# Performance work log

Hardware: AMD Instinct MI355X
Metric: run time of the kernel (lower is better)

## Reference

```python
import jax, jax.numpy as jnp
import numpy as np

B, S, D, DFF = 4, 2048, 1024, 4096
EPS = 1e-5


def layernorm(x, gamma, beta):
    mu = jnp.mean(x, axis=-1, keepdims=True)
    var = jnp.var(x, axis=-1, keepdims=True)
    return (x - mu) * jax.lax.rsqrt(var + EPS) * gamma + beta


def attention(Q, K, V, causal):
    d_k = Q.shape[-1]
    scores = jnp.einsum('bqd,bkd->bqk', Q, K) / jnp.sqrt(jnp.asarray(d_k, Q.dtype))
    if causal:
        q_len, k_len = scores.shape[-2], scores.shape[-1]
        mask = jnp.tril(jnp.ones((q_len, k_len), dtype=bool))
        scores = jnp.where(mask[None], scores, jnp.asarray(-jnp.inf, scores.dtype))
    w = jax.nn.softmax(scores, axis=-1)
    return jnp.einsum('bqk,bkd->bqd', w, V)


def setup_inputs() -> dict:
    key = jax.random.key(0)
    ks = jax.random.split(key, 12)
    sd = 0.02
    return {
        'y': jax.random.normal(ks[0], (B, S, D), jnp.float32),
        'Z': jax.random.normal(ks[1], (B, S, D), jnp.float32),
        'w1': jax.random.normal(ks[2], (D, DFF), jnp.float32) * sd,
        'b1': jnp.zeros((DFF,), jnp.float32),
        'w2': jax.random.normal(ks[3], (DFF, D), jnp.float32) * sd,
        'b2': jnp.zeros((D,), jnp.float32),
        'g1': jnp.ones((D,), jnp.float32), 'beta1': jnp.zeros((D,), jnp.float32),
        'g2': jnp.ones((D,), jnp.float32), 'beta2': jnp.zeros((D,), jnp.float32),
        'g3': jnp.ones((D,), jnp.float32), 'beta3': jnp.zeros((D,), jnp.float32),
    }


def reference(y, Z, w1, b1, w2, b2, g1, beta1, g2, beta2, g3, beta3):
    # masked (causal) self-attention, single head over full d_model
    sa = attention(y, y, y, causal=True)
    y = layernorm(y + sa, g1, beta1)
    # cross-attention to encoder memory Z
    ca = attention(y, Z, Z, causal=False)
    y = layernorm(y + ca, g2, beta2)
    # position-wise FFN
    h = jax.nn.relu(jnp.einsum('bsd,df->bsf', y, w1) + b1)
    ff = jnp.einsum('bsf,fd->bsd', h, w2) + b2
    y = layernorm(y + ff, g3, beta3)
    return y
```

## Files before the change

kernel.cpp:

```cpp
#include <hip/hip_runtime.h>
#include <hip/hip_bf16.h>


#define Bb 4
#define Ss 2048
#define Dd 1024
#define Ff 4096

typedef __attribute__((ext_vector_type(4))) float f32x4;
typedef __attribute__((ext_vector_type(8))) short bf16x8;
typedef __attribute__((ext_vector_type(8))) unsigned short u16x8;
typedef __attribute__((ext_vector_type(4))) unsigned short u16x4;

__device__ __forceinline__ unsigned short f2bf(float f) {
  unsigned u = __float_as_uint(f);
  u += 0x7FFFu + ((u >> 16) & 1u);
  return (unsigned short)(u >> 16);
}
__device__ __forceinline__ float bf2f(unsigned short h) {
  return __uint_as_float(((unsigned)h) << 16);
}

__device__ __forceinline__ void gload_lds16(const void* g, void* l) {
  __builtin_amdgcn_global_load_lds((const __attribute__((address_space(1))) void*)g,
                                   (__attribute__((address_space(3))) void*)l, 16, 0, 0);
}

__device__ __forceinline__ int xcd8(int orig, int n) {
  int q = n >> 3, r = n & 7;
  int x = orig & 7;
  int base = x < r ? x * (q + 1) : r * (q + 1) + (x - r) * q;
  return base + (orig >> 3);
}

__global__ __launch_bounds__(256) void k_transpose_cast(const float* __restrict__ in,
                                                        unsigned short* __restrict__ outT,
                                                        unsigned short* __restrict__ outR,
                                                        int R, int C) {
  __shared__ float t[32][33];
  size_t bo = (size_t)blockIdx.z * R * C;
  const float* pin = in + bo;
  unsigned short* poutT = outT + bo;
  unsigned short* poutR = outR ? outR + bo : nullptr;
  int c0 = blockIdx.x * 32, r0 = blockIdx.y * 32;
  int tx = threadIdx.x, ty = threadIdx.y;
#pragma unroll
  for (int i = 0; i < 4; i++) {
    float v = pin[(size_t)(r0 + ty + i * 8) * C + c0 + tx];
    t[ty + i * 8][tx] = v;
    if (poutR) poutR[(size_t)(r0 + ty + i * 8) * C + c0 + tx] = f2bf(v);
  }
  __syncthreads();
#pragma unroll
  for (int i = 0; i < 4; i++)
    poutT[(size_t)(c0 + ty + i * 8) * R + r0 + tx] = f2bf(t[tx][ty + i * 8]);
}

#define BAR() __builtin_amdgcn_s_barrier()
#define PRIO1() __builtin_amdgcn_s_setprio(1)
#define PRIO0() __builtin_amdgcn_s_setprio(0)
#define LGKM0()                                          \
  {                                                      \
    asm volatile("s_waitcnt lgkmcnt(0)" ::: "memory");   \
    __builtin_amdgcn_sched_barrier(0);                   \
  }

#define LDA8(arr, mh, bo)                                                       \
  {                                                                             \
    _Pragma("unroll") for (int j_ = 0; j_ < QM; ++j_) {                         \
      _Pragma("unroll") for (int kh_ = 0; kh_ < 2; ++kh_) {                     \
        arr[j_][kh_] =                                                          \
            *(const bf16x8*)(lds + (bo) + ((mh)*QM + j_) * 2048 + aof[kh_]);    \
      }                                                                         \
    }                                                                           \
  }

#define LDB8(arr, nh, bo)                                                       \
  {                                                                             \
    _Pragma("unroll") for (int n_ = 0; n_ < 2; ++n_) {                          \
      _Pragma("unroll") for (int kh_ = 0; kh_ < 2; ++kh_) {                     \
        arr[n_][kh_] =                                                          \
            *(const bf16x8*)(lds + (bo) + ((nh)*2 + n_) * 2048 + bof[kh_]);     \
      }                                                                         \
    }                                                                           \
  }

#define MMQ(aarr, barr, mh, nh)                                                 \
  {                                                                             \
    _Pragma("unroll") for (int j_ = 0; j_ < QM; ++j_) {                         \
      _Pragma("unroll") for (int n_ = 0; n_ < 2; ++n_) {                        \
        _Pragma("unroll") for (int kh_ = 0; kh_ < 2; ++kh_) {                   \
          acc[(mh)*QM + j_][(nh)*2 + n_] = __builtin_amdgcn_mfma_f32_16x16x32_bf16( \
              aarr[j_][kh_], barr[n_][kh_], acc[(mh)*QM + j_][(nh)*2 + n_], 0, 0, 0); \
        }                                                                       \
      }                                                                         \
    }                                                                           \
  }

#define EPILOGUE(MR_, WMS_)                                                     \
  {                                                                             \
    const int colb = j0 + wc * 64 + fr;                                         \
    const int rowb = i0 + wr * (WMS_) + (kq << 2);                              \
    const size_t cb = (size_t)bz * bsC;                                         \
    _Pragma("unroll") for (int m = 0; m < (MR_); ++m) {                         \
      _Pragma("unroll") for (int r = 0; r < 4; ++r) {                           \
        size_t ro = cb + (size_t)(rowb + m * 16 + r) * ldc;                     \
        _Pragma("unroll") for (int n = 0; n < 4; ++n) {                         \
          float v = acc[m][n][r];                                               \
          int col = colb + n * 16;                                              \
          if (EPI == 0) Cb[ro + col] = f2bf(v * scale);                         \
          else if (EPI == 2) Cb[ro + col] = f2bf(fmaxf(v + bias[col], 0.f));    \
          else if (EPI == 4) Cf[ro + col] = v + resid[ro + col];                \
          else Cf[ro + col] = v + bias[col] + resid[ro + col];                  \
        }                                                                       \
      }                                                                         \
    }                                                                           \
  }

template <int EPI, bool CAUSAL>
__global__ __launch_bounds__(512) void k_gemm8(
    const unsigned short* __restrict__ Ag, const unsigned short* __restrict__ Bg,
    float* __restrict__ Cf, unsigned short* __restrict__ Cb,
    const float* __restrict__ bias, const float* __restrict__ resid,
    int K, int lda, int ldb, int ldc, long bsA, long bsB, long bsC, float scale) {
  constexpr int QM = 4;
  constexpr int ABYTES = 32768, BBYTES = 32768;
  __shared__ alignas(16) char lds[2 * ABYTES + 2 * BBYTES];

  int i0, j0;
  if (CAUSAL) {
    int t = xcd8(blockIdx.x, gridDim.x);
    int ti = (int)((sqrtf(8.f * t + 1.f) - 1.f) * 0.5f);
    while ((ti + 1) * (ti + 2) / 2 <= t) ++ti;
    while (ti * (ti + 1) / 2 > t) --ti;
    i0 = ti * 256;
    j0 = (t - ti * (ti + 1) / 2) * 256;
  } else {
    int lin = xcd8(blockIdx.y * gridDim.x + blockIdx.x, gridDim.x * gridDim.y);
    i0 = (lin / gridDim.x) * 256;
    j0 = (lin % gridDim.x) * 256;
  }
  int bz = blockIdx.z;
  Ag += (size_t)bz * bsA;
  Bg += (size_t)bz * bsB;

  const int nk = K / 64;
  const int niter = nk / 2;

  const int tid = threadIdx.x;
  const int w = tid >> 6, lane = tid & 63;
  const int wr = w >> 2, wc = w & 3;

  const int srow = (w << 3) + (lane >> 3);
  const int bcs = (lane & 7) ^ (lane >> 3);
  const unsigned short* As = Ag + (size_t)(i0 + srow) * lda + bcs * 8;
  const unsigned short* Bs = Bg + (size_t)(j0 + srow) * ldb + bcs * 8;
  char* ldsAw = lds + w * 1024;
  char* ldsBw = lds + 2 * ABYTES + w * 1024;

  auto stA = [&](int kt, int hf) {
    int ks = kt < nk ? kt : nk - 1;
#pragma unroll
    for (int l = 0; l < 2; ++l)
      gload_lds16(As + (size_t)(hf * 128 + l * 64) * lda + ks * 64,
                  ldsAw + (kt & 1) * ABYTES + hf * 128 * 128 + l * 8192);
  };
  auto stB = [&](int kt, int hf) {
    int ks = kt < nk ? kt : nk - 1;
#pragma unroll
    for (int l = 0; l < 2; ++l)
      gload_lds16(Bs + (size_t)(hf * 128 + l * 64) * ldb + ks * 64,
                  ldsBw + (kt & 1) * BBYTES + hf * 128 * 128 + l * 8192);
  };

  const int fr = lane & 15, kq = lane >> 4;
  const int rA = wr * 128 + fr;
  const int rB = wc * 64 + fr;
  unsigned aof[2], bof[2];
  aof[0] = rA * 128 + ((kq ^ (rA & 7)) << 4);
  aof[1] = rA * 128 + (((kq + 4) ^ (rA & 7)) << 4);
  bof[0] = 2 * ABYTES + rB * 128 + ((kq ^ (rB & 7)) << 4);
  bof[1] = 2 * ABYTES + rB * 128 + (((kq + 4) ^ (rB & 7)) << 4);
  constexpr int A0 = 0, A1 = ABYTES, B0 = 0, B1 = BBYTES;

  f32x4 acc[8][4];
#pragma unroll
  for (int m = 0; m < 8; ++m)
#pragma unroll
    for (int n = 0; n < 4; ++n) acc[m][n] = (f32x4){0.f, 0.f, 0.f, 0.f};

  bf16x8 a0[QM][2], a1[QM][2], b0[2][2], b1[2][2];

  stA(0, 0); stA(0, 1); stB(0, 0); stB(0, 1);
  stA(1, 0); stA(1, 1); stB(1, 0);
  asm volatile("s_waitcnt vmcnt(6)" ::: "memory");
  BAR();
  LDB8(b0, 0, B0);

  for (int t = 0; t < niter; ++t) {
    const int ka = 2 * t + 2, kb = 2 * t + 3;
    LDA8(a0, 0, A0);
    stB(2 * t + 1, 1);
    BAR(); LGKM0(); PRIO1(); MMQ(a0, b0, 0, 0); PRIO0(); BAR();
    LDA8(a1, 1, A0);
    BAR(); LGKM0(); PRIO1(); MMQ(a1, b0, 1, 0); PRIO0(); BAR();
    LDB8(b1, 1, B0);
    stA(ka, 0);
    asm volatile("s_waitcnt vmcnt(2)" ::: "memory");
    BAR(); LGKM0(); PRIO1(); MMQ(a1, b1, 1, 1); PRIO0(); BAR();
    LDB8(b0, 0, B1);
    stA(ka, 1); stB(ka, 0);
    BAR(); LGKM0(); PRIO1(); MMQ(a0, b1, 0, 1); PRIO0(); BAR();
    LDA8(a0, 0, A1);
    stB(ka, 1);
    BAR(); LGKM0(); PRIO1(); MMQ(a0, b0, 0, 0); PRIO0(); BAR();
    LDA8(a1, 1, A1);
    BAR(); LGKM0(); PRIO1(); MMQ(a1, b0, 1, 0); PRIO0(); BAR();
    LDB8(b1, 1, B1);
    stA(kb, 0);
    asm volatile("s_waitcnt vmcnt(2)" ::: "memory");
    BAR(); LGKM0(); PRIO1(); MMQ(a1, b1, 1, 1); PRIO0(); BAR();
    LDB8(b0, 0, B0);
    stA(kb, 1); stB(kb, 0);
    BAR(); LGKM0(); PRIO1(); MMQ(a0, b1, 0, 1); PRIO0(); BAR();
  }
  EPILOGUE(8, 128)
}

template <int EPI, bool KCAP>
__global__ __launch_bounds__(512) void k_gemm4(
    const unsigned short* __restrict__ Ag, const unsigned short* __restrict__ Bg,
    float* __restrict__ Cf, unsigned short* __restrict__ Cb,
    const float* __restrict__ bias, const float* __restrict__ resid,
    int K, int lda, int ldb, int ldc, long bsA, long bsB, long bsC, float scale) {
  constexpr int QM = 4;
  constexpr int ABYTES = 16384, BBYTES = 32768;
  __shared__ alignas(16) char lds[2 * ABYTES + 2 * BBYTES];

  int lin = xcd8(blockIdx.y * gridDim.x + blockIdx.x, gridDim.x * gridDim.y);
  int i0 = (lin / gridDim.x) * 128;
  int j0 = (lin % gridDim.x) * 256;
  int bz = blockIdx.z;
  Ag += (size_t)bz * bsA;
  Bg += (size_t)bz * bsB;

  int nk = K / 64;
  if (KCAP) {
    int cap = i0 / 64 + 2;
    nk = nk < cap ? nk : cap;
  }
  const int niter = nk / 2;

  const int tid = threadIdx.x;
  const int w = tid >> 6, lane = tid & 63;
  const int wr = w >> 2, wc = w & 3;

  const int srow = (w << 3) + (lane >> 3);
  const int bcs = (lane & 7) ^ (lane >> 3);
  const unsigned short* As = Ag + (size_t)(i0 + srow) * lda + bcs * 8;
  const unsigned short* Bs = Bg + (size_t)(j0 + srow) * ldb + bcs * 8;
  char* ldsAw = lds + w * 1024;
  char* ldsBw = lds + 2 * ABYTES + w * 1024;

  auto stA2 = [&](int kt) {
    int ks = kt < nk ? kt : nk - 1;
#pragma unroll
    for (int hf = 0; hf < 2; ++hf)
      gload_lds16(As + (size_t)(hf * 64) * lda + ks * 64,
                  ldsAw + (kt & 1) * ABYTES + hf * 64 * 128);
  };
  auto stB2 = [&](int kt) {
    int ks = kt < nk ? kt : nk - 1;
#pragma unroll
    for (int hf = 0; hf < 2; ++hf)
#pragma unroll
      for (int l = 0; l < 2; ++l)
        gload_lds16(Bs + (size_t)(hf * 128 + l * 64) * ldb + ks * 64,
                    ldsBw + (kt & 1) * BBYTES + hf * 128 * 128 + l * 8192);
  };

  const int fr = lane & 15, kq = lane >> 4;
  const int rA = wr * 64 + fr;
  const int rB = wc * 64 + fr;
  unsigned aof[2], bof[2];
  aof[0] = rA * 128 + ((kq ^ (rA & 7)) << 4);
  aof[1] = rA * 128 + (((kq + 4) ^ (rA & 7)) << 4);
  bof[0] = 2 * ABYTES + rB * 128 + ((kq ^ (rB & 7)) << 4);
  bof[1] = 2 * ABYTES + rB * 128 + (((kq + 4) ^ (rB & 7)) << 4);
  constexpr int A0 = 0, A1 = ABYTES, B0 = 0, B1 = BBYTES;

  f32x4 acc[4][4];
#pragma unroll
  for (int m = 0; m < 4; ++m)
#pragma unroll
    for (int n = 0; n < 4; ++n) acc[m][n] = (f32x4){0.f, 0.f, 0.f, 0.f};

  bf16x8 a[QM][2], b0[2][2], b1[2][2];

  stA2(0); stB2(0); stA2(1);
  asm volatile("s_waitcnt vmcnt(2)" ::: "memory");
  BAR();

  for (int t = 0; t < niter; ++t) {
    const int ka = 2 * t + 2, kb = 2 * t + 3;
    LDA8(a, 0, A0); LDB8(b0, 0, B0);
    stB2(2 * t + 1);
    BAR(); LGKM0(); PRIO1(); MMQ(a, b0, 0, 0); PRIO0(); BAR();
    LDB8(b1, 1, B0);
    stA2(ka);
    asm volatile("s_waitcnt vmcnt(2)" ::: "memory");
    BAR(); LGKM0(); PRIO1(); MMQ(a, b1, 0, 1); PRIO0(); BAR();
    LDA8(a, 0, A1); LDB8(b0, 0, B1);
    stB2(ka);
    BAR(); LGKM0(); PRIO1(); MMQ(a, b0, 0, 0); PRIO0(); BAR();
    LDB8(b1, 1, B1);
    stA2(kb);
    asm volatile("s_waitcnt vmcnt(2)" ::: "memory");
    BAR(); LGKM0(); PRIO1(); MMQ(a, b1, 0, 1); PRIO0(); BAR();
  }
  EPILOGUE(4, 64)
}

template <bool CAUSAL>
__global__ __launch_bounds__(256) void k_softmax(unsigned short* __restrict__ scores) {
  int row = blockIdx.x;
  int i = row & (Ss - 1);
  unsigned short* src = scores + (size_t)row * Ss;
  int nv = CAUSAL ? i + 1 : Ss;
  int nb = CAUSAL ? ((i & ~127) + 128) : Ss;
  int t = threadIdx.x;
  int w = t >> 6, lane = t & 63;
  bool act = t * 8 < nb;
  float v[8];
  float mx = -1e30f;
  if (act) {
    u16x8 raw = *(const u16x8*)(src + t * 8);
#pragma unroll
    for (int k = 0; k < 8; k++) {
      int j = t * 8 + k;
      v[k] = (j < nv) ? bf2f(raw[k]) : -1e30f;
      mx = fmaxf(mx, v[k]);
    }
  } else {
#pragma unroll
    for (int k = 0; k < 8; k++) v[k] = -1e30f;
  }
#pragma unroll
  for (int o = 32; o; o >>= 1) mx = fmaxf(mx, __shfl_xor(mx, o));
  __shared__ float red[8];
  if (lane == 0) red[w] = mx;
  __syncthreads();
  mx = fmaxf(fmaxf(red[0], red[1]), fmaxf(red[2], red[3]));
  float sum = 0.f;
#pragma unroll
  for (int k = 0; k < 8; k++) {
    float e = (v[k] > -1e29f) ? __expf(v[k] - mx) : 0.f;
    v[k] = e;
    sum += e;
  }
#pragma unroll
  for (int o = 32; o; o >>= 1) sum += __shfl_xor(sum, o);
  if (lane == 0) red[4 + w] = sum;
  __syncthreads();
  sum = red[4] + red[5] + red[6] + red[7];
  float inv = 1.f / sum;
  if (act) {
    u16x8 r;
#pragma unroll
    for (int k = 0; k < 8; k++) r[k] = f2bf(v[k] * inv);
    *(u16x8*)(src + t * 8) = r;
  }
}

__global__ __launch_bounds__(256) void k_ln(const float* __restrict__ a,
                                            const float* __restrict__ g,
                                            const float* __restrict__ be,
                                            float* __restrict__ outf,
                                            unsigned short* __restrict__ outb) {
  int row = blockIdx.x;
  size_t o = (size_t)row * Dd;
  int t = threadIdx.x;
  f32x4 x = *(const f32x4*)(a + o + t * 4);
  float s = x[0] + x[1] + x[2] + x[3];
  float q = x[0] * x[0] + x[1] * x[1] + x[2] * x[2] + x[3] * x[3];
  int w = t >> 6, lane = t & 63;
#pragma unroll
  for (int of = 32; of; of >>= 1) {
    s += __shfl_xor(s, of);
    q += __shfl_xor(q, of);
  }
  __shared__ float red[8];
  if (lane == 0) {
    red[w] = s;
    red[4 + w] = q;
  }
  __syncthreads();
  s = red[0] + red[1] + red[2] + red[3];
  q = red[4] + red[5] + red[6] + red[7];
  float mean = s * (1.f / Dd);
  float var = q * (1.f / Dd) - mean * mean;
  float rstd = rsqrtf(var + 1e-5f);
  f32x4 gv = *(const f32x4*)(g + t * 4);
  f32x4 bv = *(const f32x4*)(be + t * 4);
  f32x4 y;
#pragma unroll
  for (int k = 0; k < 4; k++) y[k] = (x[k] - mean) * rstd * gv[k] + bv[k];
  *(f32x4*)(outf + o + t * 4) = y;
  if (outb) {
    u16x4 r;
    r[0] = f2bf(y[0]); r[1] = f2bf(y[1]); r[2] = f2bf(y[2]); r[3] = f2bf(y[3]);
    *(u16x4*)(outb + o + t * 4) = r;
  }
}

extern "C" void kernel_launch(void* const* d_in, const int* in_sizes, int n_in, void* d_out,
                              int out_size, void* d_ws, size_t ws_size, hipStream_t stream) {
  (void)in_sizes; (void)n_in; (void)out_size; (void)ws_size;
  const float* y   = (const float*)d_in[0];
  const float* Z   = (const float*)d_in[1];
  const float* w1  = (const float*)d_in[2];
  const float* b1  = (const float*)d_in[3];
  const float* w2  = (const float*)d_in[4];
  const float* b2  = (const float*)d_in[5];
  const float* g1  = (const float*)d_in[6];
  const float* be1 = (const float*)d_in[7];
  const float* g2  = (const float*)d_in[8];
  const float* be2 = (const float*)d_in[9];
  const float* g3  = (const float*)d_in[10];
  const float* be3 = (const float*)d_in[11];
  float* out = (float*)d_out;

  char* ws = (char*)d_ws;
  const size_t MB = 1024ull * 1024ull;
  unsigned short* T   = (unsigned short*)(ws);
  unsigned short* Zbf = (unsigned short*)(ws + 16 * MB);
  unsigned short* ybf = (unsigned short*)(ws + 32 * MB);
  unsigned short* w1t = (unsigned short*)(ws + 48 * MB);
  unsigned short* w2t = (unsigned short*)(ws + 56 * MB);
  unsigned short* sc  = (unsigned short*)(ws + 64 * MB);
  unsigned short* h   = (unsigned short*)(ws + 64 * MB);
  float* res          = (float*)(ws + 128 * MB);
  float* attn         = (float*)d_out;

  dim3 b256(256), b512(512);
  const float scl = 1.f / 32.f;

  k_transpose_cast<<<dim3(Dd / 32, Ss / 32, Bb), dim3(32, 8), 0, stream>>>(y, T, ybf, Ss, Dd);
  k_gemm8<0, true><<<dim3(36, 1, Bb), b512, 0, stream>>>(
      ybf, ybf, nullptr, sc, nullptr, nullptr, Dd, Dd, Dd, Ss,
      (long)Ss * Dd, (long)Ss * Dd, (long)Ss * Ss, scl);
  k_softmax<true><<<dim3(Bb * Ss), b256, 0, stream>>>(sc);
  k_gemm4<4, true><<<dim3(Dd / 256, Ss / 128, Bb), b512, 0, stream>>>(
      sc, T, attn, nullptr, nullptr, y, Ss, Ss, Ss, Dd,
      (long)Ss * Ss, (long)Dd * Ss, (long)Ss * Dd, 1.f);
  k_ln<<<dim3(Bb * Ss), b256, 0, stream>>>(attn, g1, be1, res, ybf);

  k_transpose_cast<<<dim3(Dd / 32, Ss / 32, Bb), dim3(32, 8), 0, stream>>>(Z, T, Zbf, Ss, Dd);
  k_gemm8<0, false><<<dim3(Ss / 256, Ss / 256, Bb), b512, 0, stream>>>(
      ybf, Zbf, nullptr, sc, nullptr, nullptr, Dd, Dd, Dd, Ss,
      (long)Ss * Dd, (long)Ss * Dd, (long)Ss * Ss, scl);
  k_softmax<false><<<dim3(Bb * Ss), b256, 0, stream>>>(sc);
  k_gemm4<4, false><<<dim3(Dd / 256, Ss / 128, Bb), b512, 0, stream>>>(
      sc, T, attn, nullptr, nullptr, res, Ss, Ss, Ss, Dd,
      (long)Ss * Ss, (long)Dd * Ss, (long)Ss * Dd, 1.f);
  k_ln<<<dim3(Bb * Ss), b256, 0, stream>>>(attn, g2, be2, res, ybf);

  k_transpose_cast<<<dim3(Ff / 32, Dd / 32, 1), dim3(32, 8), 0, stream>>>(w1, w1t, nullptr, Dd, Ff);
  k_transpose_cast<<<dim3(Dd / 32, Ff / 32, 1), dim3(32, 8), 0, stream>>>(w2, w2t, nullptr, Ff, Dd);
  k_gemm8<2, false><<<dim3(Ff / 256, (Bb * Ss) / 256, 1), b512, 0, stream>>>(
      ybf, w1t, nullptr, h, b1, nullptr, Dd, Dd, Dd, Ff, 0L, 0L, 0L, 1.f);
  k_gemm4<5, false><<<dim3(Dd / 256, (Bb * Ss) / 128, 1), b512, 0, stream>>>(
      h, w2t, attn, nullptr, b2, res, Ff, Ff, Ff, Dd, 0L, 0L, 0L, 1.f);
  k_ln<<<dim3(Bb * Ss), b256, 0, stream>>>(attn, g3, be3, out, nullptr);
}
```

Measured before the change: 396.7 us.

## Reschedule global-to-LDS prefetch in both GEMM kernels to deepen overlap

In the 8-wave GEMM, the LDS fragment loads and global-to-LDS stores are redistributed across the MFMA phases. The last phase now reuses registers already loaded and skips the LGKM wait, and the vmcnt wait moves to allow more outstanding loads. In the 4-wave GEMM, B tile staging is split into halves so the next tile's first half is issued earlier, with vmcnt thresholds adjusted to match. The goal is to hide global load latency behind matrix math. The risk is races if the waitcnt accounting is wrong, and extra register or queue pressure.

```diff
diff --git a/kernel.cpp b/kernel.cpp
--- a/kernel.cpp
+++ b/kernel.cpp
@@ -195,34 +195,33 @@
   stA(1, 0); stA(1, 1); stB(1, 0);
   asm volatile("s_waitcnt vmcnt(6)" ::: "memory");
   BAR();
-  LDB8(b0, 0, B0);
 
   for (int t = 0; t < niter; ++t) {
     const int ka = 2 * t + 2, kb = 2 * t + 3;
-    LDA8(a0, 0, A0);
+    LDA8(a0, 0, A0); LDB8(b0, 0, B0);
     stB(2 * t + 1, 1);
     BAR(); LGKM0(); PRIO1(); MMQ(a0, b0, 0, 0); PRIO0(); BAR();
     LDA8(a1, 1, A0);
+    stA(ka, 0);
     BAR(); LGKM0(); PRIO1(); MMQ(a1, b0, 1, 0); PRIO0(); BAR();
     LDB8(b1, 1, B0);
-    stA(ka, 0);
-    asm volatile("s_waitcnt vmcnt(2)" ::: "memory");
+    stA(ka, 1);
     BAR(); LGKM0(); PRIO1(); MMQ(a1, b1, 1, 1); PRIO0(); BAR();
-    LDB8(b0, 0, B1);
-    stA(ka, 1); stB(ka, 0);
-    BAR(); LGKM0(); PRIO1(); MMQ(a0, b1, 0, 1); PRIO0(); BAR();
-    LDA8(a0, 0, A1);
+    stB(ka, 0);
+    asm volatile("s_waitcnt vmcnt(6)" ::: "memory");
+    BAR(); PRIO1(); MMQ(a0, b1, 0, 1); PRIO0(); BAR();
+    LDA8(a0, 0, A1); LDB8(b0, 0, B1);
     stB(ka, 1);
     BAR(); LGKM0(); PRIO1(); MMQ(a0, b0, 0, 0); PRIO0(); BAR();
     LDA8(a1, 1, A1);
+    stA(kb, 0);
     BAR(); LGKM0(); PRIO1(); MMQ(a1, b0, 1, 0); PRIO0(); BAR();
     LDB8(b1, 1, B1);
-    stA(kb, 0);
-    asm volatile("s_waitcnt vmcnt(2)" ::: "memory");
+    stA(kb, 1);
     BAR(); LGKM0(); PRIO1(); MMQ(a1, b1, 1, 1); PRIO0(); BAR();
-    LDB8(b0, 0, B0);
-    stA(kb, 1); stB(kb, 0);
-    BAR(); LGKM0(); PRIO1(); MMQ(a0, b1, 0, 1); PRIO0(); BAR();
+    stB(kb, 0);
+    asm volatile("s_waitcnt vmcnt(6)" ::: "memory");
+    BAR(); PRIO1(); MMQ(a0, b1, 0, 1); PRIO0(); BAR();
   }
   EPILOGUE(8, 128)
 }
@@ -269,14 +268,12 @@
       gload_lds16(As + (size_t)(hf * 64) * lda + ks * 64,
                   ldsAw + (kt & 1) * ABYTES + hf * 64 * 128);
   };
-  auto stB2 = [&](int kt) {
+  auto stBh = [&](int kt, int hf) {
     int ks = kt < nk ? kt : nk - 1;
 #pragma unroll
-    for (int hf = 0; hf < 2; ++hf)
-#pragma unroll
-      for (int l = 0; l < 2; ++l)
-        gload_lds16(Bs + (size_t)(hf * 128 + l * 64) * ldb + ks * 64,
-                    ldsBw + (kt & 1) * BBYTES + hf * 128 * 128 + l * 8192);
+    for (int l = 0; l < 2; ++l)
+      gload_lds16(Bs + (size_t)(hf * 128 + l * 64) * ldb + ks * 64,
+                  ldsBw + (kt & 1) * BBYTES + hf * 128 * 128 + l * 8192);
   };
 
   const int fr = lane & 15, kq = lane >> 4;
@@ -297,25 +294,26 @@
 
   bf16x8 a[QM][2], b0[2][2], b1[2][2];
 
-  stA2(0); stB2(0); stA2(1);
-  asm volatile("s_waitcnt vmcnt(2)" ::: "memory");
+  stA2(0); stBh(0, 0); stBh(0, 1);
+  stA2(1); stBh(1, 0);
+  asm volatile("s_waitcnt vmcnt(4)" ::: "memory");
   BAR();
 
   for (int t = 0; t < niter; ++t) {
     const int ka = 2 * t + 2, kb = 2 * t + 3;
     LDA8(a, 0, A0); LDB8(b0, 0, B0);
-    stB2(2 * t + 1);
+    stBh(2 * t + 1, 1);
     BAR(); LGKM0(); PRIO1(); MMQ(a, b0, 0, 0); PRIO0(); BAR();
     LDB8(b1, 1, B0);
-    stA2(ka);
-    asm volatile("s_waitcnt vmcnt(2)" ::: "memory");
+    stA2(ka); stBh(ka, 0);
+    asm volatile("s_waitcnt vmcnt(4)" ::: "memory");
     BAR(); LGKM0(); PRIO1(); MMQ(a, b1, 0, 1); PRIO0(); BAR();
     LDA8(a, 0, A1); LDB8(b0, 0, B1);
-    stB2(ka);
+    stBh(ka, 1);
     BAR(); LGKM0(); PRIO1(); MMQ(a, b0, 0, 0); PRIO0(); BAR();
     LDB8(b1, 1, B1);
-    stA2(kb);
-    asm volatile("s_waitcnt vmcnt(2)" ::: "memory");
+    stA2(kb); stBh(kb, 0);
+    asm volatile("s_waitcnt vmcnt(4)" ::: "memory");
     BAR(); LGKM0(); PRIO1(); MMQ(a, b1, 0, 1); PRIO0(); BAR();
   }
   EPILOGUE(4, 64)
```

After: 393.6 us. About the same (-0.8%).
